# Optimization experiments

Hardware: AMD Instinct MI355X
Metric: run time of the kernel (lower is better)

Reference implementation:

```python
import jax, jax.numpy as jnp
import numpy as np

N_HEAD = 16
N_KV = 4
HEAD_DIM = 128
N_EMBD = 2048
GATE_CH = 32


def setup_inputs() -> dict:
    key = jax.random.key(0)
    ks = jax.random.split(key, 9)
    B, T = 2, 2048
    return {
        "x": jax.random.normal(ks[0], (B, T, N_EMBD), jnp.float32),
        "ve": jax.random.normal(ks[1], (B, T, N_KV * HEAD_DIM), jnp.float32),
        "cos": jax.random.uniform(ks[2], (T, 1, HEAD_DIM // 2), jnp.float32),
        "sin": jax.random.uniform(ks[3], (T, 1, HEAD_DIM // 2), jnp.float32),
        "wq": jax.random.normal(ks[4], (N_HEAD * HEAD_DIM, N_EMBD), jnp.float32) * 0.02,
        "wk": jax.random.normal(ks[5], (N_KV * HEAD_DIM, N_EMBD), jnp.float32) * 0.02,
        "wv": jax.random.normal(ks[6], (N_KV * HEAD_DIM, N_EMBD), jnp.float32) * 0.02,
        "wo": jax.random.normal(ks[7], (N_EMBD, N_EMBD), jnp.float32) * 0.02,
        "wgate": jax.random.normal(ks[8], (N_KV, GATE_CH), jnp.float32) * 0.02,
        "window_size": 512,
    }


def _rope(t, cos, sin):
    half = t.shape[-1] // 2
    t1, t2 = t[..., :half], t[..., half:]
    return jnp.concatenate([t1 * cos + t2 * sin, -t1 * sin + t2 * cos], axis=-1)


def _rms(t):
    eps = jnp.finfo(t.dtype).eps
    return t * jax.lax.rsqrt(jnp.mean(t * t, axis=-1, keepdims=True) + eps)


def reference(x, ve, cos, sin, wq, wk, wv, wo, wgate, window_size):
    B, T, _ = x.shape
    q = (x @ wq.T).reshape(B, T, N_HEAD, HEAD_DIM)
    k = (x @ wk.T).reshape(B, T, N_KV, HEAD_DIM)
    v = (x @ wv.T).reshape(B, T, N_KV, HEAD_DIM)
    # value-embedding gate
    gate = 2.0 * jax.nn.sigmoid(x[..., :GATE_CH] @ wgate.T)  # [B,T,N_KV]
    v = v + gate[..., None] * ve.reshape(B, T, N_KV, HEAD_DIM)
    # RoPE then QK RMSNorm
    q = _rms(_rope(q, cos, sin)).transpose(0, 2, 1, 3)  # [B,H,T,D]
    k = _rms(_rope(k, cos, sin)).transpose(0, 2, 1, 3)  # [B,KV,T,D]
    v = v.transpose(0, 2, 1, 3)
    rep = N_HEAD // N_KV
    k = jnp.repeat(k, rep, axis=1)  # repeat_interleave over head dim
    v = jnp.repeat(v, rep, axis=1)
    # sliding-window causal mask (past_len=0, key_len=T)
    pos = jnp.arange(T)
    mask = (pos[None, :] <= pos[:, None]) & (pos[None, :] >= pos[:, None] - window_size + 1)
    scale = 1.0 / jnp.sqrt(jnp.float32(HEAD_DIM))
    scores = jnp.einsum("bhqd,bhkd->bhqk", q, k) * scale
    scores = jnp.where(mask[None, None], scores, jnp.finfo(scores.dtype).min)
    attn = jax.nn.softmax(scores, axis=-1)
    y = jnp.einsum("bhqk,bhkd->bhqd", attn, v)
    y = y.transpose(0, 2, 1, 3).reshape(B, T, N_EMBD)
    return y @ wo.T
```

## Files before the change

### kernel.cpp

```cpp
#include <hip/hip_runtime.h>
#include <hip/hip_bf16.h>

typedef __attribute__((ext_vector_type(8))) short short8_t;
typedef __attribute__((ext_vector_type(4))) float f32x4;
typedef __attribute__((ext_vector_type(16))) float f32x16;
using bf16 = __hip_bfloat16;

#define MFMA_BF16(A, B, C) __builtin_amdgcn_mfma_f32_16x16x32_bf16((A), (B), (C), 0, 0, 0)
#define MFMA32_BF16(A, B, C) __builtin_amdgcn_mfma_f32_32x32x16_bf16((A), (B), (C), 0, 0, 0)

#define GLD_LDS16(g, l)                                                        \
  __builtin_amdgcn_global_load_lds(                                           \
      (const __attribute__((address_space(1))) unsigned int*)(const void*)(g),\
      (__attribute__((address_space(3))) unsigned int*)(void*)(l), 16, 0, 0)

__device__ __forceinline__ float bits2f(short s) {
  union { unsigned int u; float f; } c;
  c.u = ((unsigned int)(unsigned short)s) << 16;
  return c.f;
}
__device__ __forceinline__ short f2bits(float f) {
  bf16 h = __float2bfloat16(f);
  return *reinterpret_cast<short*>(&h);
}
__device__ __forceinline__ unsigned pack2(float lo, float hi) {
  return ((unsigned)(unsigned short)f2bits(lo)) |
         (((unsigned)(unsigned short)f2bits(hi)) << 16);
}
__device__ __forceinline__ float exp2_(float x) {
#if __has_builtin(__builtin_amdgcn_exp2f)
  return __builtin_amdgcn_exp2f(x);
#else
  return exp2f(x);
#endif
}

__global__ __launch_bounds__(256) void cvt_f32_bf16(const float* __restrict__ in,
                                                    short* __restrict__ out, int n) {
  int i = (blockIdx.x * 256 + threadIdx.x) * 4;
  if (i >= n) return;
  float4 v = *reinterpret_cast<const float4*>(in + i);
  short4 o;
  o.x = f2bits(v.x); o.y = f2bits(v.y); o.z = f2bits(v.z); o.w = f2bits(v.w);
  *reinterpret_cast<short4*>(out + i) = o;
}

__global__ __launch_bounds__(256) void cvt_w3(const float* __restrict__ wq,
                                              const float* __restrict__ wk,
                                              const float* __restrict__ wv,
                                              short* __restrict__ out) {
  int i = (blockIdx.x * 256 + threadIdx.x) * 4;
  const float* src;
  int off;
  if (i < 4194304) { src = wq; off = i; }
  else if (i < 5242880) { src = wk; off = i - 4194304; }
  else { src = wv; off = i - 5242880; }
  float4 v = *reinterpret_cast<const float4*>(src + off);
  short4 o;
  o.x = f2bits(v.x); o.y = f2bits(v.y); o.z = f2bits(v.z); o.w = f2bits(v.w);
  *reinterpret_cast<short4*>(out + i) = o;
}

template <int STORE_BF16>
__global__ __launch_bounds__(256, 2) void gemm_bt4(const short* __restrict__ A,
                                                   const short* __restrict__ Bt,
                                                   void* __restrict__ C,
                                                   int M, int N, int K, int NBN) {
  __shared__ __align__(16) short lds[2 * 16384];
  const int nwg = gridDim.x;
  const int cpx = nwg >> 3;
  const int wg = ((int)blockIdx.x & 7) * cpx + ((int)blockIdx.x >> 3);
  const int m0 = (wg / NBN) * 128, n0 = (wg % NBN) * 128;

  const int tid = threadIdx.x, w = tid >> 6, lane = tid & 63;
  const int wr = w >> 1, wc = w & 1;
  const int rr = lane & 15, g = lane >> 4;

  const int srow = tid >> 3;
  const int gc = (tid & 7) ^ (srow & 7);
  const short* Asrc = A + (size_t)(m0 + srow) * K + gc * 8;
  const short* Bsrc = Bt + (size_t)(n0 + srow) * K + gc * 8;
  const size_t rstep = (size_t)32 * K;
  const int dofs = tid * 16;

  const int abase = (((wr * 64 + rr) << 7) | (g << 4)) ^ ((rr & 7) << 4);
  const int bbase = ((((wc * 64 + rr) << 7) | (g << 4)) ^ ((rr & 7) << 4)) + 16384;

  f32x4 acc[4][4];
#pragma unroll
  for (int mi = 0; mi < 4; ++mi)
#pragma unroll
    for (int ni = 0; ni < 4; ++ni) acc[mi][ni] = (f32x4){0.f, 0.f, 0.f, 0.f};

  const int nt = K >> 6;

#define STAGE4(t, bufbyte) do {                                                \
    const short* a_ = Asrc + (size_t)(t) * 64;                                 \
    const short* b_ = Bsrc + (size_t)(t) * 64;                                 \
    char* la_ = (char*)lds + (bufbyte) + dofs;                                 \
    GLD_LDS16(a_,             la_);                                            \
    GLD_LDS16(a_ + rstep,     la_ + 4096);                                     \
    GLD_LDS16(a_ + 2 * rstep, la_ + 8192);                                     \
    GLD_LDS16(a_ + 3 * rstep, la_ + 12288);                                    \
    GLD_LDS16(b_,             la_ + 16384);                                    \
    GLD_LDS16(b_ + rstep,     la_ + 20480);                                    \
    GLD_LDS16(b_ + 2 * rstep, la_ + 24576);                                    \
    GLD_LDS16(b_ + 3 * rstep, la_ + 28672);                                    \
  } while (0)

  STAGE4(0, 0);
  asm volatile("s_waitcnt vmcnt(0)" ::: "memory");
  asm volatile("s_barrier" ::: "memory");

  int cur = 0;
  for (int t = 0; t < nt; ++t) {
    if (t + 1 < nt) STAGE4(t + 1, cur ^ 32768);
    const char* bufp = (const char*)lds + cur;
#pragma unroll
    for (int kk = 0; kk < 2; ++kk) {
      const int ko = kk * 64;
      short8_t a0 = *(const short8_t*)(bufp + ((abase ^ ko)));
      short8_t a1 = *(const short8_t*)(bufp + ((abase ^ ko) + 2048));
      short8_t a2 = *(const short8_t*)(bufp + ((abase ^ ko) + 4096));
      short8_t a3 = *(const short8_t*)(bufp + ((abase ^ ko) + 6144));
      short8_t b0 = *(const short8_t*)(bufp + ((bbase ^ ko)));
      short8_t b1 = *(const short8_t*)(bufp + ((bbase ^ ko) + 2048));
      short8_t b2 = *(const short8_t*)(bufp + ((bbase ^ ko) + 4096));
      short8_t b3 = *(const short8_t*)(bufp + ((bbase ^ ko) + 6144));
      __builtin_amdgcn_s_setprio(1);
      acc[0][0] = MFMA_BF16(a0, b0, acc[0][0]);
      acc[0][1] = MFMA_BF16(a0, b1, acc[0][1]);
      acc[0][2] = MFMA_BF16(a0, b2, acc[0][2]);
      acc[0][3] = MFMA_BF16(a0, b3, acc[0][3]);
      acc[1][0] = MFMA_BF16(a1, b0, acc[1][0]);
      acc[1][1] = MFMA_BF16(a1, b1, acc[1][1]);
      acc[1][2] = MFMA_BF16(a1, b2, acc[1][2]);
      acc[1][3] = MFMA_BF16(a1, b3, acc[1][3]);
      acc[2][0] = MFMA_BF16(a2, b0, acc[2][0]);
      acc[2][1] = MFMA_BF16(a2, b1, acc[2][1]);
      acc[2][2] = MFMA_BF16(a2, b2, acc[2][2]);
      acc[2][3] = MFMA_BF16(a2, b3, acc[2][3]);
      acc[3][0] = MFMA_BF16(a3, b0, acc[3][0]);
      acc[3][1] = MFMA_BF16(a3, b1, acc[3][1]);
      acc[3][2] = MFMA_BF16(a3, b2, acc[3][2]);
      acc[3][3] = MFMA_BF16(a3, b3, acc[3][3]);
      __builtin_amdgcn_s_setprio(0);
    }
    if (t + 1 < nt) {
      asm volatile("s_waitcnt vmcnt(0)" ::: "memory");
      asm volatile("s_barrier" ::: "memory");
    }
    cur ^= 32768;
  }
#undef STAGE4

#pragma unroll
  for (int mi = 0; mi < 4; ++mi)
#pragma unroll
    for (int ni = 0; ni < 4; ++ni) {
      const int row = m0 + wr * 64 + mi * 16 + g * 4;
      const int col = n0 + wc * 64 + ni * 16 + rr;
#pragma unroll
      for (int j = 0; j < 4; ++j) {
        float v = acc[mi][ni][j];
        if (STORE_BF16)
          reinterpret_cast<short*>(C)[(size_t)(row + j) * N + col] = f2bits(v);
        else
          reinterpret_cast<float*>(C)[(size_t)(row + j) * N + col] = v;
      }
    }
}

__global__ __launch_bounds__(256) void rope_rms_qk(const short* __restrict__ qkv,
                                                   const float* __restrict__ cosT,
                                                   const float* __restrict__ sinT,
                                                   short* __restrict__ qO,
                                                   short* __restrict__ kO) {
  const int T = 2048;
  int unit = blockIdx.x * 4 + (threadIdx.x >> 6);
  int lane = threadIdx.x & 63;
  int hh = unit % 20;
  int t = (unit / 20) % T;
  int b = unit / (20 * T);
  int col = hh < 16 ? hh * 128 : 2048 + (hh - 16) * 128;
  const short* src = qkv + (size_t)(b * T + t) * 3072 + col;
  float t1 = bits2f(src[lane]), t2 = bits2f(src[lane + 64]);
  float c = cosT[t * 64 + lane], s = sinT[t * 64 + lane];
  float o1 = t1 * c + t2 * s;
  float o2 = t2 * c - t1 * s;
  float ss = o1 * o1 + o2 * o2;
#pragma unroll
  for (int o = 1; o < 64; o <<= 1) ss += __shfl_xor(ss, o, 64);
  float r = rsqrtf(ss * (1.f / 128.f) + 1.1920929e-07f);
  short* dst;
  if (hh < 16) {
    r *= 0.08838834764831845f * 1.4426950408889634f;
    dst = qO + ((size_t)(b * 16 + hh) * T + t) * 128;
  } else {
    dst = kO + ((size_t)(b * 4 + (hh - 16)) * T + t) * 128;
  }
  dst[lane] = f2bits(o1 * r);
  dst[lane + 64] = f2bits(o2 * r);
}

__global__ __launch_bounds__(256) void v_gate(const short* __restrict__ qkv,
                                              const float* __restrict__ x,
                                              const float* __restrict__ ve,
                                              const float* __restrict__ wgate,
                                              short* __restrict__ vO) {
  const int T = 2048;
  int unit = blockIdx.x * 4 + (threadIdx.x >> 6);
  int lane = threadIdx.x & 63;
  int kv = unit & 3;
  int t = (unit >> 2) % T;
  int b = unit / (4 * T);
  size_t m = (size_t)b * T + t;
  float z = 0.f;
  if (lane < 32) z = x[m * 2048 + lane] * wgate[kv * 32 + lane];
#pragma unroll
  for (int o = 1; o < 64; o <<= 1) z += __shfl_xor(z, o, 64);
  float gate = 2.f / (1.f + __expf(-z));
  const short* vsrc = qkv + m * 3072 + 2560 + kv * 128;
  const float* vesrc = ve + m * 512 + kv * 128;
  short* dst = vO + ((size_t)(b * 4 + kv) * T + t) * 128;
  dst[lane] = f2bits(bits2f(vsrc[lane]) + gate * vesrc[lane]);
  dst[lane + 64] = f2bits(bits2f(vsrc[lane + 64]) + gate * vesrc[lane + 64]);
}

__global__ __launch_bounds__(256) void v_transpose(const short* __restrict__ vp,
                                                   short* __restrict__ vT) {
  const int T = 2048;
  int bkv = blockIdx.x & 7;
  int t0 = (blockIdx.x >> 3) * 64;
  __shared__ __align__(16) short L[128 * 64];
  int tid = threadIdx.x;
  int tt = tid >> 2, dblk = tid & 3;
  const short* src = vp + ((size_t)bkv * T + t0 + tt) * 128 + dblk * 32;
  short8_t v0 = *(const short8_t*)(src);
  short8_t v1 = *(const short8_t*)(src + 8);
  short8_t v2 = *(const short8_t*)(src + 16);
  short8_t v3 = *(const short8_t*)(src + 24);
#pragma unroll
  for (int i = 0; i < 32; ++i) {
    int d = dblk * 32 + i;
    int byte = (d * 128 + tt * 2) ^ ((d & 7) << 4);
    short val = i < 8 ? v0[i] : i < 16 ? v1[i - 8] : i < 24 ? v2[i - 16] : v3[i - 24];
    *(short*)((char*)L + byte) = val;
  }
  __syncthreads();
  int d = tid >> 1, th = tid & 1;
  short* dst = vT + ((size_t)bkv * 128 + d) * T + t0 + th * 64;
  const char* Lp = (const char*)L;
#pragma unroll
  for (int g2 = 0; g2 < 4; ++g2) {
    short8_t o = *(const short8_t*)(Lp + ((d * 128 + th * 64 + g2 * 16) ^ ((d & 7) << 4)));
    *(short8_t*)(vT + ((size_t)bkv * 128 + d) * T + t0 + th * 32 + g2 * 8) = o;
  }
  (void)dst;
}

__global__ __launch_bounds__(256) void attn_sw3(const short* __restrict__ Q,
                                                const short* __restrict__ K,
                                                const short* __restrict__ VT,
                                                short* __restrict__ Y,
                                                const int* __restrict__ winp) {
  const int T = 2048, H = 16;
  const int win = *winp;
  int combo = blockIdx.x & 7;
  int j = blockIdx.x >> 3;
  int b = combo >> 2, kvh = combo & 3;
  int h = kvh * 4 + (j & 3);
  int q0 = (15 - (j >> 2)) * 128;

  __shared__ __align__(16) short Ks[2][64 * 128];
  __shared__ __align__(16) short Vs[2][128 * 64];

  int tid = threadIdx.x, w = tid >> 6, lane = tid & 63;
  int ql = lane & 31, hi = lane >> 5;
  int qrow = q0 + w * 32 + ql;

  const short* qbase = Q + ((size_t)(b * H + h) * T + qrow) * 128;
  short8_t qf[8];
#pragma unroll
  for (int ks = 0; ks < 8; ++ks)
    qf[ks] = *reinterpret_cast<const short8_t*>(qbase + ks * 16 + hi * 8);

  const short* kbase = K + (size_t)(b * 4 + kvh) * T * 128;
  const short* vtbase = VT + (size_t)(b * 4 + kvh) * 128 * T;

  f32x16 acc[4];
#pragma unroll
  for (int dt = 0; dt < 4; ++dt)
#pragma unroll
    for (int r = 0; r < 16; ++r) acc[dt][r] = 0.f;
  float mreg = -1e30f, lsum = 0.f;

  int lo = q0 - win + 1;
  if (lo < 0) lo = 0;
  lo &= ~63;
  const int nt = (q0 + 128 - lo) >> 6;
  int qmin = q0 + w * 32, qmax = qmin + 31;

#define STAGE_A(ti, bi) do {                                                   \
    int kc_ = lo + (ti) * 64;                                                  \
    _Pragma("unroll")                                                          \
    for (int r = 0; r < 4; ++r) {                                              \
      int slot = (r * 4 + w) * 64 + lane;                                      \
      int krow = slot >> 4;                                                    \
      int gc = (slot & 15) ^ (krow & 7);                                       \
      GLD_LDS16(kbase + (size_t)(kc_ + krow) * 128 + gc * 8,                   \
                (char*)Ks[bi] + (r * 4 + w) * 1024);                           \
    }                                                                          \
    _Pragma("unroll")                                                          \
    for (int r = 0; r < 4; ++r) {                                              \
      int slot = (r * 4 + w) * 64 + lane;                                      \
      int d_ = slot >> 3;                                                      \
      int gc = (slot & 7) ^ (d_ & 7);                                          \
      GLD_LDS16(vtbase + (size_t)d_ * T + kc_ + gc * 8,                        \
                (char*)Vs[bi] + (r * 4 + w) * 1024);                           \
    }                                                                          \
  } while (0)

  STAGE_A(0, 0);

  int cur = 0;
  for (int t = 0; t < nt; ++t) {
    if (t + 1 < nt) {
      STAGE_A(t + 1, cur ^ 1);
      asm volatile("s_waitcnt vmcnt(8)" ::: "memory");
    } else {
      asm volatile("s_waitcnt vmcnt(0)" ::: "memory");
    }
    asm volatile("s_barrier" ::: "memory");

    int kc = lo + t * 64;
    bool active = (kc <= qmax) && (kc + 63 >= qmin - win + 1);
    if (active) {
      const char* Kp = (const char*)Ks[cur];
      const char* Vp = (const char*)Vs[cur];
      f32x16 sA[2];
#pragma unroll
      for (int r = 0; r < 16; ++r) { sA[0][r] = 0.f; sA[1][r] = 0.f; }
#pragma unroll
      for (int kt = 0; kt < 2; ++kt) {
        int kr = kt * 32 + ql;
#pragma unroll
        for (int ks = 0; ks < 8; ++ks) {
          int byte = kr * 256 + (((ks * 2 + hi) ^ (kr & 7)) << 4);
          short8_t kf = *reinterpret_cast<const short8_t*>(Kp + byte);
          sA[kt] = MFMA32_BF16(kf, qf[ks], sA[kt]);
        }
      }
      float pmax = -1e30f;
#pragma unroll
      for (int kt = 0; kt < 2; ++kt)
#pragma unroll
        for (int r = 0; r < 16; ++r) {
          int key = kc + kt * 32 + (r & 3) + 8 * (r >> 2) + 4 * hi;
          float sv = sA[kt][r];
          sv = ((unsigned)(qrow - key) < (unsigned)win) ? sv : -1e30f;
          sA[kt][r] = sv;
          pmax = fmaxf(pmax, sv);
        }
      pmax = fmaxf(pmax, __shfl_xor(pmax, 32, 64));
      float mn = fmaxf(mreg, pmax);
      float corr = exp2_(mreg - mn);
      mreg = mn;
      float rs = 0.f;
#pragma unroll
      for (int kt = 0; kt < 2; ++kt)
#pragma unroll
        for (int r = 0; r < 16; ++r) {
          float p = exp2_(sA[kt][r] - mn);
          sA[kt][r] = p;
          rs += p;
        }
      rs += __shfl_xor(rs, 32, 64);
      lsum = lsum * corr + rs;
#pragma unroll
      for (int dt = 0; dt < 4; ++dt)
#pragma unroll
        for (int r = 0; r < 16; ++r) acc[dt][r] *= corr;

#pragma unroll
      for (int kt = 0; kt < 2; ++kt)
#pragma unroll
        for (int s = 0; s < 2; ++s) {
          unsigned a = pack2(sA[kt][8 * s + 0], sA[kt][8 * s + 1]);
          unsigned bb = pack2(sA[kt][8 * s + 2], sA[kt][8 * s + 3]);
          unsigned c = pack2(sA[kt][8 * s + 4], sA[kt][8 * s + 5]);
          unsigned dd = pack2(sA[kt][8 * s + 6], sA[kt][8 * s + 7]);
          unsigned sa = __shfl_xor(a, 32, 64);
          unsigned sb = __shfl_xor(bb, 32, 64);
          unsigned sc2 = __shfl_xor(c, 32, 64);
          unsigned sd = __shfl_xor(dd, 32, 64);
          union { unsigned u[4]; short8_t s8; } pu;
          pu.u[0] = hi ? sc2 : a;
          pu.u[1] = hi ? sd : bb;
          pu.u[2] = hi ? c : sa;
          pu.u[3] = hi ? dd : sb;
          const int kst = kt * 2 + s;
#pragma unroll
          for (int dt = 0; dt < 4; ++dt) {
            int d_ = dt * 32 + ql;
            int byte = (d_ << 7) + ((((kst * 2 + hi)) ^ (d_ & 7)) << 4);
            short8_t vf = *reinterpret_cast<const short8_t*>(Vp + byte);
            acc[dt] = MFMA32_BF16(vf, pu.s8, acc[dt]);
          }
        }
    }
    asm volatile("s_barrier" ::: "memory");
    cur ^= 1;
  }
#undef STAGE_A

  float rinv = 1.f / lsum;
  short* ybase = Y + ((size_t)(b * T + qrow) * H + h) * 128;
#pragma unroll
  for (int dt = 0; dt < 4; ++dt)
#pragma unroll
    for (int g2 = 0; g2 < 4; ++g2) {
      short4 o;
      o.x = f2bits(acc[dt][g2 * 4 + 0] * rinv);
      o.y = f2bits(acc[dt][g2 * 4 + 1] * rinv);
      o.z = f2bits(acc[dt][g2 * 4 + 2] * rinv);
      o.w = f2bits(acc[dt][g2 * 4 + 3] * rinv);
      *reinterpret_cast<short4*>(ybase + dt * 32 + 8 * g2 + 4 * hi) = o;
    }
}

extern "C" void kernel_launch(void* const* d_in, const int* in_sizes, int n_in,
                              void* d_out, int out_size, void* d_ws, size_t ws_size,
                              hipStream_t stream) {
  const float* x = (const float*)d_in[0];
  const float* ve = (const float*)d_in[1];
  const float* cosT = (const float*)d_in[2];
  const float* sinT = (const float*)d_in[3];
  const float* wq = (const float*)d_in[4];
  const float* wk = (const float*)d_in[5];
  const float* wv = (const float*)d_in[6];
  const float* wo = (const float*)d_in[7];
  const float* wgate = (const float*)d_in[8];
  const int* winp = (const int*)d_in[9];
  float* out = (float*)d_out;
  char* ws = (char*)d_ws;

  const int B = 2, T = 2048;
  short* xb    = (short*)(ws);
  short* wqkvb = (short*)(ws + 16777216);
  short* wob   = (short*)(ws + 29360128);
  short* qkv   = (short*)(ws + 37748736);
  short* qpost = (short*)(ws + 62914560);
  short* kpost = (short*)(ws + 79691776);
  short* vpost = (short*)(ws + 83886080);
  short* ybuf  = (short*)(ws + 88080384);
  short* vTb   = qkv;

  cvt_f32_bf16<<<dim3(8192), 256, 0, stream>>>(x, xb, B * T * 2048);
  cvt_w3<<<dim3(6144), 256, 0, stream>>>(wq, wk, wv, wqkvb);
  cvt_f32_bf16<<<dim3(4096), 256, 0, stream>>>(wo, wob, 2048 * 2048);

  gemm_bt4<1><<<dim3(768), 256, 0, stream>>>(xb, wqkvb, qkv, 4096, 3072, 2048, 24);

  rope_rms_qk<<<dim3(B * T * 20 / 4), 256, 0, stream>>>(qkv, cosT, sinT, qpost, kpost);
  v_gate<<<dim3(B * T), 256, 0, stream>>>(qkv, x, ve, wgate, vpost);
  v_transpose<<<dim3(8 * (T / 64)), 256, 0, stream>>>(vpost, vTb);

  attn_sw3<<<dim3(512), 256, 0, stream>>>(qpost, kpost, vTb, ybuf, winp);

  gemm_bt4<0><<<dim3(512), 256, 0, stream>>>(ybuf, wob, out, 4096, 2048, 2048, 16);
}
```

Before: 185.8 us.

## Rewrite GEMM as 2-wave 128x128 tile with triple-buffered K=32 pipeline

Replaces the 4-wave, double-buffered, K=64-step GEMM with a 2-wave kernel in which each wave computes a 128x64 sub-tile (8x4 MFMA accumulators) over K=32 steps, using three LDS buffers so two global-to-LDS loads stay in flight. Fragment loads are issued before the next stage's prefetch, and partial vmcnt waits replace full drains, to overlap memory with MFMA work and raise per-wave operand reuse. The cost is more accumulator registers per wave, fewer waves per block, and a barrier every 32-wide K step. Both the QKV and output projections now use this kernel.

```diff
diff --git a/kernel.cpp b/kernel.cpp
--- a/kernel.cpp
+++ b/kernel.cpp
@@ -62,104 +62,126 @@
 }
 
 template <int STORE_BF16>
-__global__ __launch_bounds__(256, 2) void gemm_bt4(const short* __restrict__ A,
+__global__ __launch_bounds__(128, 2) void gemm_bt5(const short* __restrict__ A,
                                                    const short* __restrict__ Bt,
                                                    void* __restrict__ C,
                                                    int M, int N, int K, int NBN) {
-  __shared__ __align__(16) short lds[2 * 16384];
+  __shared__ __align__(16) short lds[3 * 8192];
   const int nwg = gridDim.x;
   const int cpx = nwg >> 3;
   const int wg = ((int)blockIdx.x & 7) * cpx + ((int)blockIdx.x >> 3);
   const int m0 = (wg / NBN) * 128, n0 = (wg % NBN) * 128;
 
   const int tid = threadIdx.x, w = tid >> 6, lane = tid & 63;
-  const int wr = w >> 1, wc = w & 1;
   const int rr = lane & 15, g = lane >> 4;
 
-  const int srow = tid >> 3;
-  const int gc = (tid & 7) ^ (srow & 7);
-  const short* Asrc = A + (size_t)(m0 + srow) * K + gc * 8;
-  const short* Bsrc = Bt + (size_t)(n0 + srow) * K + gc * 8;
-  const size_t rstep = (size_t)32 * K;
+  const int srow = tid >> 2;
+  const int sg = (tid & 3) ^ (srow & 3);
+  const short* Asrc = A + (size_t)(m0 + srow) * K + sg * 8;
+  const short* Bsrc = Bt + (size_t)(n0 + srow) * K + sg * 8;
   const int dofs = tid * 16;
 
-  const int abase = (((wr * 64 + rr) << 7) | (g << 4)) ^ ((rr & 7) << 4);
-  const int bbase = ((((wc * 64 + rr) << 7) | (g << 4)) ^ ((rr & 7) << 4)) + 16384;
-
-  f32x4 acc[4][4];
-#pragma unroll
-  for (int mi = 0; mi < 4; ++mi)
+  const int xorg = ((g ^ (rr & 3)) << 4);
+  const int abase = rr * 64 + xorg;
+  const int bbase = 8192 + w * 4096 + rr * 64 + xorg;
+
+  f32x4 acc[8][4];
+#pragma unroll
+  for (int mi = 0; mi < 8; ++mi)
 #pragma unroll
     for (int ni = 0; ni < 4; ++ni) acc[mi][ni] = (f32x4){0.f, 0.f, 0.f, 0.f};
 
-  const int nt = K >> 6;
-
-#define STAGE4(t, bufbyte) do {                                                \
-    const short* a_ = Asrc + (size_t)(t) * 64;                                 \
-    const short* b_ = Bsrc + (size_t)(t) * 64;                                 \
-    char* la_ = (char*)lds + (bufbyte) + dofs;                                 \
-    GLD_LDS16(a_,             la_);                                            \
-    GLD_LDS16(a_ + rstep,     la_ + 4096);                                     \
-    GLD_LDS16(a_ + 2 * rstep, la_ + 8192);                                     \
-    GLD_LDS16(a_ + 3 * rstep, la_ + 12288);                                    \
-    GLD_LDS16(b_,             la_ + 16384);                                    \
-    GLD_LDS16(b_ + rstep,     la_ + 20480);                                    \
-    GLD_LDS16(b_ + 2 * rstep, la_ + 24576);                                    \
-    GLD_LDS16(b_ + 3 * rstep, la_ + 28672);                                    \
+  const int ns = K >> 5;
+
+#define STG5(s_, base_) do {                                                   \
+    const short* a_ = Asrc + (size_t)(s_) * 32;                                \
+    const short* b_ = Bsrc + (size_t)(s_) * 32;                                \
+    char* d_ = (char*)lds + (base_) + dofs;                                    \
+    GLD_LDS16(a_,                  d_);                                        \
+    GLD_LDS16(a_ + (size_t)32 * K, d_ + 2048);                                 \
+    GLD_LDS16(a_ + (size_t)64 * K, d_ + 4096);                                 \
+    GLD_LDS16(a_ + (size_t)96 * K, d_ + 6144);                                 \
+    GLD_LDS16(b_,                  d_ + 8192);                                 \
+    GLD_LDS16(b_ + (size_t)32 * K, d_ + 10240);                                \
+    GLD_LDS16(b_ + (size_t)64 * K, d_ + 12288);                                \
+    GLD_LDS16(b_ + (size_t)96 * K, d_ + 14336);                                \
   } while (0)
 
-  STAGE4(0, 0);
-  asm volatile("s_waitcnt vmcnt(0)" ::: "memory");
+  STG5(0, 0);
+  if (ns > 1) STG5(1, 16384);
+  asm volatile("s_waitcnt vmcnt(8)" ::: "memory");
   asm volatile("s_barrier" ::: "memory");
 
-  int cur = 0;
-  for (int t = 0; t < nt; ++t) {
-    if (t + 1 < nt) STAGE4(t + 1, cur ^ 32768);
-    const char* bufp = (const char*)lds + cur;
-#pragma unroll
-    for (int kk = 0; kk < 2; ++kk) {
-      const int ko = kk * 64;
-      short8_t a0 = *(const short8_t*)(bufp + ((abase ^ ko)));
-      short8_t a1 = *(const short8_t*)(bufp + ((abase ^ ko) + 2048));
-      short8_t a2 = *(const short8_t*)(bufp + ((abase ^ ko) + 4096));
-      short8_t a3 = *(const short8_t*)(bufp + ((abase ^ ko) + 6144));
-      short8_t b0 = *(const short8_t*)(bufp + ((bbase ^ ko)));
-      short8_t b1 = *(const short8_t*)(bufp + ((bbase ^ ko) + 2048));
-      short8_t b2 = *(const short8_t*)(bufp + ((bbase ^ ko) + 4096));
-      short8_t b3 = *(const short8_t*)(bufp + ((bbase ^ ko) + 6144));
-      __builtin_amdgcn_s_setprio(1);
-      acc[0][0] = MFMA_BF16(a0, b0, acc[0][0]);
-      acc[0][1] = MFMA_BF16(a0, b1, acc[0][1]);
-      acc[0][2] = MFMA_BF16(a0, b2, acc[0][2]);
-      acc[0][3] = MFMA_BF16(a0, b3, acc[0][3]);
-      acc[1][0] = MFMA_BF16(a1, b0, acc[1][0]);
-      acc[1][1] = MFMA_BF16(a1, b1, acc[1][1]);
-      acc[1][2] = MFMA_BF16(a1, b2, acc[1][2]);
-      acc[1][3] = MFMA_BF16(a1, b3, acc[1][3]);
-      acc[2][0] = MFMA_BF16(a2, b0, acc[2][0]);
-      acc[2][1] = MFMA_BF16(a2, b1, acc[2][1]);
-      acc[2][2] = MFMA_BF16(a2, b2, acc[2][2]);
-      acc[2][3] = MFMA_BF16(a2, b3, acc[2][3]);
-      acc[3][0] = MFMA_BF16(a3, b0, acc[3][0]);
-      acc[3][1] = MFMA_BF16(a3, b1, acc[3][1]);
-      acc[3][2] = MFMA_BF16(a3, b2, acc[3][2]);
-      acc[3][3] = MFMA_BF16(a3, b3, acc[3][3]);
-      __builtin_amdgcn_s_setprio(0);
-    }
-    if (t + 1 < nt) {
+  int c0 = 0, c1 = 16384, c2 = 32768;
+  for (int s = 0; s < ns; ++s) {
+    const char* bufp = (const char*)lds + c0;
+    short8_t a0 = *(const short8_t*)(bufp + abase);
+    short8_t a1 = *(const short8_t*)(bufp + abase + 1024);
+    short8_t a2 = *(const short8_t*)(bufp + abase + 2048);
+    short8_t a3 = *(const short8_t*)(bufp + abase + 3072);
+    short8_t a4 = *(const short8_t*)(bufp + abase + 4096);
+    short8_t a5 = *(const short8_t*)(bufp + abase + 5120);
+    short8_t a6 = *(const short8_t*)(bufp + abase + 6144);
+    short8_t a7 = *(const short8_t*)(bufp + abase + 7168);
+    short8_t b0 = *(const short8_t*)(bufp + bbase);
+    short8_t b1 = *(const short8_t*)(bufp + bbase + 1024);
+    short8_t b2 = *(const short8_t*)(bufp + bbase + 2048);
+    short8_t b3 = *(const short8_t*)(bufp + bbase + 3072);
+
+    if (s + 2 < ns) STG5(s + 2, c2);
+
+    asm volatile("s_waitcnt lgkmcnt(0)" ::: "memory");
+    __builtin_amdgcn_sched_barrier(0);
+    __builtin_amdgcn_s_setprio(1);
+    acc[0][0] = MFMA_BF16(a0, b0, acc[0][0]);
+    acc[0][1] = MFMA_BF16(a0, b1, acc[0][1]);
+    acc[0][2] = MFMA_BF16(a0, b2, acc[0][2]);
+    acc[0][3] = MFMA_BF16(a0, b3, acc[0][3]);
+    acc[1][0] = MFMA_BF16(a1, b0, acc[1][0]);
+    acc[1][1] = MFMA_BF16(a1, b1, acc[1][1]);
+    acc[1][2] = MFMA_BF16(a1, b2, acc[1][2]);
+    acc[1][3] = MFMA_BF16(a1, b3, acc[1][3]);
+    acc[2][0] = MFMA_BF16(a2, b0, acc[2][0]);
+    acc[2][1] = MFMA_BF16(a2, b1, acc[2][1]);
+    acc[2][2] = MFMA_BF16(a2, b2, acc[2][2]);
+    acc[2][3] = MFMA_BF16(a2, b3, acc[2][3]);
+    acc[3][0] = MFMA_BF16(a3, b0, acc[3][0]);
+    acc[3][1] = MFMA_BF16(a3, b1, acc[3][1]);
+    acc[3][2] = MFMA_BF16(a3, b2, acc[3][2]);
+    acc[3][3] = MFMA_BF16(a3, b3, acc[3][3]);
+    acc[4][0] = MFMA_BF16(a4, b0, acc[4][0]);
+    acc[4][1] = MFMA_BF16(a4, b1, acc[4][1]);
+    acc[4][2] = MFMA_BF16(a4, b2, acc[4][2]);
+    acc[4][3] = MFMA_BF16(a4, b3, acc[4][3]);
+    acc[5][0] = MFMA_BF16(a5, b0, acc[5][0]);
+    acc[5][1] = MFMA_BF16(a5, b1, acc[5][1]);
+    acc[5][2] = MFMA_BF16(a5, b2, acc[5][2]);
+    acc[5][3] = MFMA_BF16(a5, b3, acc[5][3]);
+    acc[6][0] = MFMA_BF16(a6, b0, acc[6][0]);
+    acc[6][1] = MFMA_BF16(a6, b1, acc[6][1]);
+    acc[6][2] = MFMA_BF16(a6, b2, acc[6][2]);
+    acc[6][3] = MFMA_BF16(a6, b3, acc[6][3]);
+    acc[7][0] = MFMA_BF16(a7, b0, acc[7][0]);
+    acc[7][1] = MFMA_BF16(a7, b1, acc[7][1]);
+    acc[7][2] = MFMA_BF16(a7, b2, acc[7][2]);
+    acc[7][3] = MFMA_BF16(a7, b3, acc[7][3]);
+    __builtin_amdgcn_s_setprio(0);
+
+    if (s + 2 < ns)
+      asm volatile("s_waitcnt vmcnt(8)" ::: "memory");
+    else if (s + 1 < ns)
       asm volatile("s_waitcnt vmcnt(0)" ::: "memory");
-      asm volatile("s_barrier" ::: "memory");
-    }
-    cur ^= 32768;
+    asm volatile("s_barrier" ::: "memory");
+    int t_ = c0; c0 = c1; c1 = c2; c2 = t_;
   }
-#undef STAGE4
-
-#pragma unroll
-  for (int mi = 0; mi < 4; ++mi)
+#undef STG5
+
+#pragma unroll
+  for (int mi = 0; mi < 8; ++mi)
 #pragma unroll
     for (int ni = 0; ni < 4; ++ni) {
-      const int row = m0 + wr * 64 + mi * 16 + g * 4;
-      const int col = n0 + wc * 64 + ni * 16 + rr;
+      const int row = m0 + mi * 16 + g * 4;
+      const int col = n0 + w * 64 + ni * 16 + rr;
 #pragma unroll
       for (int j = 0; j < 4; ++j) {
         float v = acc[mi][ni][j];
@@ -249,14 +271,12 @@
   }
   __syncthreads();
   int d = tid >> 1, th = tid & 1;
-  short* dst = vT + ((size_t)bkv * 128 + d) * T + t0 + th * 64;
   const char* Lp = (const char*)L;
 #pragma unroll
   for (int g2 = 0; g2 < 4; ++g2) {
     short8_t o = *(const short8_t*)(Lp + ((d * 128 + th * 64 + g2 * 16) ^ ((d & 7) << 4)));
     *(short8_t*)(vT + ((size_t)bkv * 128 + d) * T + t0 + th * 32 + g2 * 8) = o;
   }
-  (void)dst;
 }
 
 __global__ __launch_bounds__(256) void attn_sw3(const short* __restrict__ Q,
@@ -460,7 +480,7 @@
   cvt_w3<<<dim3(6144), 256, 0, stream>>>(wq, wk, wv, wqkvb);
   cvt_f32_bf16<<<dim3(4096), 256, 0, stream>>>(wo, wob, 2048 * 2048);
 
-  gemm_bt4<1><<<dim3(768), 256, 0, stream>>>(xb, wqkvb, qkv, 4096, 3072, 2048, 24);
+  gemm_bt5<1><<<dim3(768), 128, 0, stream>>>(xb, wqkvb, qkv, 4096, 3072, 2048, 24);
 
   rope_rms_qk<<<dim3(B * T * 20 / 4), 256, 0, stream>>>(qkv, cosT, sinT, qpost, kpost);
   v_gate<<<dim3(B * T), 256, 0, stream>>>(qkv, x, ve, wgate, vpost);
@@ -468,5 +488,5 @@
 
   attn_sw3<<<dim3(512), 256, 0, stream>>>(qpost, kpost, vTb, ybuf, winp);
 
-  gemm_bt4<0><<<dim3(512), 256, 0, stream>>>(ybuf, wob, out, 4096, 2048, 2048, 16);
-}
+  gemm_bt5<0><<<dim3(512), 128, 0, stream>>>(ybuf, wob, out, 4096, 2048, 2048, 16);
+}
```

New measurement: 197.3 us. 1.06x slower.

## Fuse conversion kernels, merge V gate with transpose, remap GEMM tiles per XCD

Applied to the files above, without the earlier changes.

Merges the three f32-to-bf16 conversion launches into one kernel. Fuses the value-embedding gate into the V transpose kernel, which removes the intermediate vpost buffer write and reread and one launch. Changes the GEMM workgroup-to-tile mapping so each of the 8 XCDs gets a contiguous 2D block of tiles (4 along M by 2 along N), aiming for better L2 reuse of A and B. The vT buffer moves to its own workspace slot instead of aliasing qkv, which vgate_t still reads.

```diff
diff --git a/kernel.cpp b/kernel.cpp
--- a/kernel.cpp
+++ b/kernel.cpp
@@ -35,42 +35,47 @@
 #endif
 }
 
-__global__ __launch_bounds__(256) void cvt_f32_bf16(const float* __restrict__ in,
-                                                    short* __restrict__ out, int n) {
+__global__ __launch_bounds__(256) void cvt_all(const float* __restrict__ x,
+                                               const float* __restrict__ wq,
+                                               const float* __restrict__ wk,
+                                               const float* __restrict__ wv,
+                                               const float* __restrict__ wo,
+                                               short* __restrict__ xb,
+                                               short* __restrict__ wqkvb,
+                                               short* __restrict__ wob) {
   int i = (blockIdx.x * 256 + threadIdx.x) * 4;
-  if (i >= n) return;
-  float4 v = *reinterpret_cast<const float4*>(in + i);
+  const float* src;
+  short* dst;
+  if (i < 8388608) {
+    src = x + i; dst = xb + i;
+  } else if (i < 14680064) {
+    int j = i - 8388608;
+    dst = wqkvb + j;
+    if (j < 4194304) src = wq + j;
+    else if (j < 5242880) src = wk + (j - 4194304);
+    else src = wv + (j - 5242880);
+  } else {
+    int j = i - 14680064;
+    src = wo + j; dst = wob + j;
+  }
+  float4 v = *reinterpret_cast<const float4*>(src);
   short4 o;
   o.x = f2bits(v.x); o.y = f2bits(v.y); o.z = f2bits(v.z); o.w = f2bits(v.w);
-  *reinterpret_cast<short4*>(out + i) = o;
-}
-
-__global__ __launch_bounds__(256) void cvt_w3(const float* __restrict__ wq,
-                                              const float* __restrict__ wk,
-                                              const float* __restrict__ wv,
-                                              short* __restrict__ out) {
-  int i = (blockIdx.x * 256 + threadIdx.x) * 4;
-  const float* src;
-  int off;
-  if (i < 4194304) { src = wq; off = i; }
-  else if (i < 5242880) { src = wk; off = i - 4194304; }
-  else { src = wv; off = i - 5242880; }
-  float4 v = *reinterpret_cast<const float4*>(src + off);
-  short4 o;
-  o.x = f2bits(v.x); o.y = f2bits(v.y); o.z = f2bits(v.z); o.w = f2bits(v.w);
-  *reinterpret_cast<short4*>(out + i) = o;
+  *reinterpret_cast<short4*>(dst) = o;
 }
 
 template <int STORE_BF16>
 __global__ __launch_bounds__(256, 2) void gemm_bt4(const short* __restrict__ A,
                                                    const short* __restrict__ Bt,
                                                    void* __restrict__ C,
-                                                   int M, int N, int K, int NBN) {
+                                                   int M, int N, int K,
+                                                   int CM, int CN) {
   __shared__ __align__(16) short lds[2 * 16384];
-  const int nwg = gridDim.x;
-  const int cpx = nwg >> 3;
-  const int wg = ((int)blockIdx.x & 7) * cpx + ((int)blockIdx.x >> 3);
-  const int m0 = (wg / NBN) * 128, n0 = (wg % NBN) * 128;
+  const int c = (int)blockIdx.x & 7;
+  const int i = (int)blockIdx.x >> 3;
+  const int cmi = c & 3, cni = c >> 2;
+  const int m0 = (cmi * CM + (i % CM)) * 128;
+  const int n0 = (cni * CN + (i / CM)) * 128;
 
   const int tid = threadIdx.x, w = tid >> 6, lane = tid & 63;
   const int wr = w >> 1, wc = w & 1;
@@ -203,60 +208,52 @@
   dst[lane + 64] = f2bits(o2 * r);
 }
 
-__global__ __launch_bounds__(256) void v_gate(const short* __restrict__ qkv,
-                                              const float* __restrict__ x,
-                                              const float* __restrict__ ve,
-                                              const float* __restrict__ wgate,
-                                              short* __restrict__ vO) {
-  const int T = 2048;
-  int unit = blockIdx.x * 4 + (threadIdx.x >> 6);
-  int lane = threadIdx.x & 63;
-  int kv = unit & 3;
-  int t = (unit >> 2) % T;
-  int b = unit / (4 * T);
-  size_t m = (size_t)b * T + t;
-  float z = 0.f;
-  if (lane < 32) z = x[m * 2048 + lane] * wgate[kv * 32 + lane];
-#pragma unroll
-  for (int o = 1; o < 64; o <<= 1) z += __shfl_xor(z, o, 64);
-  float gate = 2.f / (1.f + __expf(-z));
-  const short* vsrc = qkv + m * 3072 + 2560 + kv * 128;
-  const float* vesrc = ve + m * 512 + kv * 128;
-  short* dst = vO + ((size_t)(b * 4 + kv) * T + t) * 128;
-  dst[lane] = f2bits(bits2f(vsrc[lane]) + gate * vesrc[lane]);
-  dst[lane + 64] = f2bits(bits2f(vsrc[lane + 64]) + gate * vesrc[lane + 64]);
-}
-
-__global__ __launch_bounds__(256) void v_transpose(const short* __restrict__ vp,
-                                                   short* __restrict__ vT) {
+__global__ __launch_bounds__(256) void vgate_t(const short* __restrict__ qkv,
+                                               const float* __restrict__ x,
+                                               const float* __restrict__ ve,
+                                               const float* __restrict__ wgate,
+                                               short* __restrict__ vT) {
   const int T = 2048;
   int bkv = blockIdx.x & 7;
   int t0 = (blockIdx.x >> 3) * 64;
+  int b = bkv >> 2, kv = bkv & 3;
   __shared__ __align__(16) short L[128 * 64];
   int tid = threadIdx.x;
-  int tt = tid >> 2, dblk = tid & 3;
-  const short* src = vp + ((size_t)bkv * T + t0 + tt) * 128 + dblk * 32;
-  short8_t v0 = *(const short8_t*)(src);
-  short8_t v1 = *(const short8_t*)(src + 8);
-  short8_t v2 = *(const short8_t*)(src + 16);
-  short8_t v3 = *(const short8_t*)(src + 24);
+  int tt = tid >> 2, q = tid & 3;
+  size_t m = (size_t)b * T + t0 + tt;
+  float z = 0.f;
+  const float* xp = x + m * 2048 + q * 8;
+  const float* wgp = wgate + kv * 32 + q * 8;
+#pragma unroll
+  for (int i = 0; i < 8; ++i) z += xp[i] * wgp[i];
+  z += __shfl_xor(z, 1, 64);
+  z += __shfl_xor(z, 2, 64);
+  float gate = 2.f / (1.f + __expf(-z));
+  const short* vsrc = qkv + m * 3072 + 2560 + kv * 128 + q * 32;
+  const float* vesrc = ve + m * 512 + kv * 128 + q * 32;
+  short8_t v0 = *(const short8_t*)(vsrc);
+  short8_t v1 = *(const short8_t*)(vsrc + 8);
+  short8_t v2 = *(const short8_t*)(vsrc + 16);
+  short8_t v3 = *(const short8_t*)(vsrc + 24);
+  float4 e[8];
+#pragma unroll
+  for (int i = 0; i < 8; ++i) e[i] = *(const float4*)(vesrc + i * 4);
 #pragma unroll
   for (int i = 0; i < 32; ++i) {
-    int d = dblk * 32 + i;
+    int d = q * 32 + i;
+    short vv = i < 8 ? v0[i] : i < 16 ? v1[i - 8] : i < 24 ? v2[i - 16] : v3[i - 24];
+    float ev = (&e[i >> 2].x)[i & 3];
     int byte = (d * 128 + tt * 2) ^ ((d & 7) << 4);
-    short val = i < 8 ? v0[i] : i < 16 ? v1[i - 8] : i < 24 ? v2[i - 16] : v3[i - 24];
-    *(short*)((char*)L + byte) = val;
+    *(short*)((char*)L + byte) = f2bits(bits2f(vv) + gate * ev);
   }
   __syncthreads();
   int d = tid >> 1, th = tid & 1;
-  short* dst = vT + ((size_t)bkv * 128 + d) * T + t0 + th * 64;
   const char* Lp = (const char*)L;
 #pragma unroll
   for (int g2 = 0; g2 < 4; ++g2) {
     short8_t o = *(const short8_t*)(Lp + ((d * 128 + th * 64 + g2 * 16) ^ ((d & 7) << 4)));
     *(short8_t*)(vT + ((size_t)bkv * 128 + d) * T + t0 + th * 32 + g2 * 8) = o;
   }
-  (void)dst;
 }
 
 __global__ __launch_bounds__(256) void attn_sw3(const short* __restrict__ Q,
@@ -452,21 +449,17 @@
   short* qkv   = (short*)(ws + 37748736);
   short* qpost = (short*)(ws + 62914560);
   short* kpost = (short*)(ws + 79691776);
-  short* vpost = (short*)(ws + 83886080);
+  short* vTb   = (short*)(ws + 83886080);
   short* ybuf  = (short*)(ws + 88080384);
-  short* vTb   = qkv;
-
-  cvt_f32_bf16<<<dim3(8192), 256, 0, stream>>>(x, xb, B * T * 2048);
-  cvt_w3<<<dim3(6144), 256, 0, stream>>>(wq, wk, wv, wqkvb);
-  cvt_f32_bf16<<<dim3(4096), 256, 0, stream>>>(wo, wob, 2048 * 2048);
-
-  gemm_bt4<1><<<dim3(768), 256, 0, stream>>>(xb, wqkvb, qkv, 4096, 3072, 2048, 24);
+
+  cvt_all<<<dim3(18432), 256, 0, stream>>>(x, wq, wk, wv, wo, xb, wqkvb, wob);
+
+  gemm_bt4<1><<<dim3(768), 256, 0, stream>>>(xb, wqkvb, qkv, 4096, 3072, 2048, 8, 12);
 
   rope_rms_qk<<<dim3(B * T * 20 / 4), 256, 0, stream>>>(qkv, cosT, sinT, qpost, kpost);
-  v_gate<<<dim3(B * T), 256, 0, stream>>>(qkv, x, ve, wgate, vpost);
-  v_transpose<<<dim3(8 * (T / 64)), 256, 0, stream>>>(vpost, vTb);
+  vgate_t<<<dim3(8 * (T / 64)), 256, 0, stream>>>(qkv, x, ve, wgate, vTb);
 
   attn_sw3<<<dim3(512), 256, 0, stream>>>(qpost, kpost, vTb, ybuf, winp);
 
-  gemm_bt4<0><<<dim3(512), 256, 0, stream>>>(ybuf, wob, out, 4096, 2048, 2048, 16);
-}
+  gemm_bt4<0><<<dim3(512), 256, 0, stream>>>(ybuf, wob, out, 4096, 2048, 2048, 8, 8);
+}
```

After: 176.5 us. -5.0%, faster.
